# Kernel optimization log

Measured on AMD Instinct MI355X. Metric: run time of the kernel, lower is better.

The kernel has to match this reference:

```python
import jax, jax.numpy as jnp
import numpy as np


def setup_inputs() -> dict:
    key = jax.random.key(0)
    ks = jax.random.split(key, 8)
    B, C, H, W = 4, 256, 64, 64
    Ci = C // 8  # inter_channels = 32
    x = jax.random.normal(ks[0], (B, C, H, W), dtype=jnp.float32)
    # 1x1 conv weights stored as [out, in] matrices (kernel size 1)
    sq = 1.0 / np.sqrt(C)
    Wq = jax.random.uniform(ks[1], (Ci, C), jnp.float32, -sq, sq)
    bq = jax.random.uniform(ks[2], (Ci,), jnp.float32, -sq, sq)
    Wk = jax.random.uniform(ks[3], (Ci, C), jnp.float32, -sq, sq)
    bk = jax.random.uniform(ks[4], (Ci,), jnp.float32, -sq, sq)
    Wv = jax.random.uniform(ks[5], (C, C), jnp.float32, -sq, sq)
    bv = jax.random.uniform(ks[6], (C,), jnp.float32, -sq, sq)
    # torch initializes gamma to zeros; use a nonzero value so output depends on attention path
    gamma = jnp.array([0.5], dtype=jnp.float32)
    return {"x": x, "Wq": Wq, "bq": bq, "Wk": Wk, "bk": bk, "Wv": Wv, "bv": bv, "gamma": gamma}


def reference(x, Wq, bq, Wk, bk, Wv, bv, gamma):
    B, C, H, W = x.shape
    N = H * W
    xf = x.reshape(B, C, N)                        # [B, C, N]
    # 1x1 convs == channel-mixing matmuls
    q = jnp.einsum('oc,bcn->bon', Wq, xf) + bq[None, :, None]   # [B, Ci, N]
    k = jnp.einsum('oc,bcn->bon', Wk, xf) + bk[None, :, None]   # [B, Ci, N]
    v = jnp.einsum('oc,bcn->bon', Wv, xf) + bv[None, :, None]   # [B, C,  N]
    # energy[b, n, m] = sum_c q[b, c, n] * k[b, c, m]  (no scaling, per DANet)
    energy = jnp.einsum('bcn,bcm->bnm', q, k)      # [B, N, N]
    attention = jax.nn.softmax(energy, axis=-1)    # softmax over keys m
    # out[b, c, n] = sum_m v[b, c, m] * attention[b, n, m]
    out = jnp.einsum('bcm,bnm->bcn', v, attention)
    out = out.reshape(B, C, H, W)
    return gamma[0] * out + x
```

## Files before the change

kernel.cpp:

```cpp
#include <hip/hip_runtime.h>
#include <hip/hip_bf16.h>
#include <math.h>

typedef __bf16 bf16x8 __attribute__((ext_vector_type(8)));
typedef float  floatx4 __attribute__((ext_vector_type(4)));
typedef float  floatx16 __attribute__((ext_vector_type(16)));
typedef unsigned u32x2 __attribute__((ext_vector_type(2)));

#define MFMA(a, b, c)   __builtin_amdgcn_mfma_f32_16x16x32_bf16((a), (b), (c), 0, 0, 0)
#define MFMA32(a, b, c) __builtin_amdgcn_mfma_f32_32x32x16_bf16((a), (b), (c), 0, 0, 0)

__device__ __forceinline__ unsigned short f2bf(float f) {
  union { float f; unsigned u; } v; v.f = f;
  unsigned r = v.u + 0x7FFFu + ((v.u >> 16) & 1u);
  return (unsigned short)(r >> 16);
}
__device__ __forceinline__ float bf2f(unsigned short u) {
  union { unsigned u; float f; } v; v.u = ((unsigned)u) << 16;
  return v.f;
}
__device__ __forceinline__ unsigned pack2(float a, float b) {
  __bf16 x = (__bf16)a, y = (__bf16)b;
  unsigned short ux = __builtin_bit_cast(unsigned short, x);
  unsigned short uy = __builtin_bit_cast(unsigned short, y);
  return (unsigned)ux | ((unsigned)uy << 16);
}
__device__ __forceinline__ float exp2_fast(float x) {
#if __has_builtin(__builtin_amdgcn_exp2f)
  return __builtin_amdgcn_exp2f(x);
#else
  return exp2f(x);
#endif
}

__global__ __launch_bounds__(256) void k_wconv(const float* __restrict__ Wq,
                                               const float* __restrict__ Wk,
                                               const float* __restrict__ Wv,
                                               unsigned short* __restrict__ Wall) {
  int i = blockIdx.x * 256 + threadIdx.x;
  int o = i >> 8, c = i & 255;
  float v = (o < 32) ? Wq[o * 256 + c]
          : (o < 64) ? Wk[(o - 32) * 256 + c]
                     : Wv[(o - 64) * 256 + c];
  Wall[i] = f2bf(v);
}

__global__ __launch_bounds__(256) void k_xpose(const float* __restrict__ x,
                                               unsigned short* __restrict__ xT) {
  int bid = blockIdx.x;
  int b = bid >> 8, rem = bid & 255;
  int nb = rem >> 2, cb = rem & 3;
  int n0 = nb * 64, c0 = cb * 64;
  int tid = threadIdx.x;
  __shared__ alignas(16) unsigned short T[64][72];
#pragma unroll
  for (int i = 0; i < 4; ++i) {
    int idx = tid + 256 * i;
    int r = idx >> 4, g = idx & 15;
    float4 d = *(const float4*)(x + ((size_t)b * 256 + c0 + r) * 4096 + n0 + g * 4);
    T[g * 4 + 0][r] = f2bf(d.x);
    T[g * 4 + 1][r] = f2bf(d.y);
    T[g * 4 + 2][r] = f2bf(d.z);
    T[g * 4 + 3][r] = f2bf(d.w);
  }
  __syncthreads();
#pragma unroll
  for (int i = 0; i < 2; ++i) {
    int idx = tid + 256 * i;
    int j = idx >> 3, g = idx & 7;
    *(uint4*)(xT + ((size_t)b * 4096 + n0 + j) * 256 + c0 + g * 8) =
        *(const uint4*)&T[j][g * 8];
  }
}

__global__ __launch_bounds__(64, 4) void k_proj(const unsigned short* __restrict__ xT,
                                                const unsigned short* __restrict__ Wall,
                                                const float* __restrict__ bq,
                                                const float* __restrict__ bk,
                                                const float* __restrict__ bv,
                                                unsigned short* __restrict__ qbf,
                                                unsigned short* __restrict__ kbf,
                                                unsigned short* __restrict__ vbf) {
  int b = blockIdx.x >> 9;
  int m0 = ((blockIdx.x >> 1) & 255) * 16;
  int h = blockIdx.x & 1;
  int lane = threadIdx.x & 63;
  int l15 = lane & 15, quad = lane >> 4;

  floatx4 acc[10];
#pragma unroll
  for (int tt = 0; tt < 10; ++tt) acc[tt] = floatx4{0.f, 0.f, 0.f, 0.f};

  const unsigned short* arow = xT + ((size_t)b * 4096 + m0 + l15) * 256;
#pragma unroll
  for (int ks = 0; ks < 8; ++ks) {
    bf16x8 a = *(const bf16x8*)(arow + ks * 32 + quad * 8);
#pragma unroll
    for (int tt = 0; tt < 10; ++tt) {
      int gt = (tt < 2) ? (h * 2 + tt) : (4 + h * 8 + (tt - 2));
      bf16x8 w = *(const bf16x8*)(Wall + (size_t)(gt * 16 + l15) * 256 + ks * 32 + quad * 8);
      acc[tt] = MFMA(a, w, acc[tt]);
    }
  }
#pragma unroll
  for (int tt = 0; tt < 2; ++tt) {
    int o = (h * 2 + tt) * 16 + l15;
    float bias = (o < 32) ? bq[o] : bk[o - 32];
    float scale = (o < 32) ? 1.44269504088896340736f : 1.0f;
    unsigned short* dst = (o < 32) ? qbf : kbf;
    int oc = o & 31;
    int kh = oc >> 4, h2 = (oc >> 3) & 1, c8 = oc & 7;
#pragma unroll
    for (int r = 0; r < 4; ++r) {
      int m = m0 + quad * 4 + r;
      dst[(size_t)b * 131072 + (size_t)(m >> 5) * 1024 + kh * 512 + h2 * 256 +
          (m & 31) * 8 + c8] = f2bf((acc[tt][r] + bias) * scale);
    }
  }
  __shared__ alignas(16) unsigned short Os[128][24];
#pragma unroll
  for (int tt = 2; tt < 10; ++tt) {
    int lr = (tt - 2) * 16 + l15;
    int c = h * 128 + lr;
    float bias = bv[c];
#pragma unroll
    for (int r = 0; r < 4; ++r)
      Os[lr][quad * 4 + r] = f2bf(acc[tt][r] + bias);
  }
  __syncthreads();
  {
    int kb = m0 >> 5, kk = (m0 >> 4) & 1;
#pragma unroll
    for (int i = 0; i < 4; ++i) {
      int idx = threadIdx.x + 64 * i;
      int cbl = idx >> 6;
      int rem = idx & 63;
      int h2 = rem >> 5, ch = rem & 31;
      int r = cbl * 32 + ch;
      *(uint4*)(vbf + (size_t)b * 1048576 + (size_t)kb * 8192 +
                (size_t)(h * 4 + cbl) * 1024 + kk * 512 + h2 * 256 + ch * 8) =
          *(const uint4*)&Os[r][h2 * 8];
    }
  }
}

__device__ __forceinline__ void softmax_pack(floatx16 st, float& lp, bf16x8 (&pa)[2], int hi) {
  float p[16];
#pragma unroll
  for (int r = 0; r < 16; ++r) p[r] = exp2_fast(st[r]);
  lp += (((p[0] + p[1]) + (p[2] + p[3])) + ((p[4] + p[5]) + (p[6] + p[7]))) +
        (((p[8] + p[9]) + (p[10] + p[11])) + ((p[12] + p[13]) + (p[14] + p[15])));
  unsigned d0[4], d1[4];
#pragma unroll
  for (int t = 0; t < 4; ++t) {
    d0[t] = pack2(p[4 * t + 0], p[4 * t + 1]);
    d1[t] = pack2(p[4 * t + 2], p[4 * t + 3]);
  }
#pragma unroll
  for (int ks = 0; ks < 2; ++ks) {
#if __has_builtin(__builtin_amdgcn_permlane32_swap)
    (void)hi;
    u32x2 r0 = __builtin_amdgcn_permlane32_swap(d0[2 * ks], d0[2 * ks + 1], false, false);
    u32x2 r1 = __builtin_amdgcn_permlane32_swap(d1[2 * ks], d1[2 * ks + 1], false, false);
    union { unsigned u[4]; bf16x8 v; } u;
    u.u[0] = r0[0]; u.u[1] = r1[0]; u.u[2] = r0[1]; u.u[3] = r1[1];
    pa[ks] = u.v;
#else
    unsigned s0 = hi ? d0[2 * ks] : d0[2 * ks + 1];
    unsigned s1 = hi ? d1[2 * ks] : d1[2 * ks + 1];
    unsigned o0 = (unsigned)__shfl_xor((int)s0, 32);
    unsigned o1 = (unsigned)__shfl_xor((int)s1, 32);
    union { unsigned u[4]; bf16x8 v; } u;
    u.u[0] = hi ? o0 : d0[2 * ks];
    u.u[1] = hi ? o1 : d1[2 * ks];
    u.u[2] = hi ? d0[2 * ks + 1] : o0;
    u.u[3] = hi ? d1[2 * ks + 1] : o1;
    pa[ks] = u.v;
#endif
  }
}

__global__ __launch_bounds__(64, 2) void k_attn(const unsigned short* __restrict__ qbf,
                                                const unsigned short* __restrict__ kbf,
                                                const unsigned short* __restrict__ vbf,
                                                unsigned short* __restrict__ Obf,
                                                float* __restrict__ lsum) {
  int wg = (blockIdx.x & 7) * 256 + (blockIdx.x >> 3);
  const int qb = wg & 63;
  const int g  = wg >> 6;
  const int cw = g & 1;
  const int s  = (g >> 1) & 3;
  const int b  = g >> 3;
  const int lane = threadIdx.x & 63;
  const int l31 = lane & 31;
  const int hi  = lane >> 5;
  const int q0  = qb * 64;

  const floatx16 z16 = {0.f, 0.f, 0.f, 0.f, 0.f, 0.f, 0.f, 0.f,
                        0.f, 0.f, 0.f, 0.f, 0.f, 0.f, 0.f, 0.f};

  bf16x8 qf[2][2];
  {
    const unsigned short* qbase =
        qbf + (size_t)b * 131072 + (size_t)(qb * 2) * 1024 + hi * 256 + l31 * 8;
#pragma unroll
    for (int qs2 = 0; qs2 < 2; ++qs2)
#pragma unroll
      for (int kh = 0; kh < 2; ++kh)
        qf[qs2][kh] = *(const bf16x8*)(qbase + qs2 * 1024 + kh * 512);
  }

  floatx16 acc[2][4];
#pragma unroll
  for (int i = 0; i < 2; ++i)
#pragma unroll
    for (int j = 0; j < 4; ++j) acc[i][j] = z16;

  float lp0 = 0.f, lp1 = 0.f;

  const unsigned short* krow =
      kbf + (size_t)b * 131072 + (size_t)(s * 32) * 1024 + hi * 256 + l31 * 8;
  const unsigned short* vrow =
      vbf + (size_t)b * 1048576 + (size_t)(s * 32) * 8192 + (size_t)(cw * 4) * 1024 +
      hi * 256 + l31 * 8;

  bf16x8 kf0 = *(const bf16x8*)krow;
  bf16x8 kf1 = *(const bf16x8*)(krow + 512);
  floatx16 st0 = MFMA32(kf0, qf[0][0], z16);
  st0 = MFMA32(kf1, qf[0][1], st0);
  floatx16 st1 = MFMA32(kf0, qf[1][0], z16);
  st1 = MFMA32(kf1, qf[1][1], st1);
  kf0 = *(const bf16x8*)(krow + 1024);
  kf1 = *(const bf16x8*)(krow + 1024 + 512);

  for (int it = 0; it < 32; ++it) {
    bf16x8 vb[4][2];
    const unsigned short* vit = vrow + (size_t)it * 8192;
#pragma unroll
    for (int ct = 0; ct < 4; ++ct) {
      vb[ct][0] = *(const bf16x8*)(vit + ct * 1024);
      vb[ct][1] = *(const bf16x8*)(vit + ct * 1024 + 512);
    }

    bf16x8 pa[2][2];
    softmax_pack(st0, lp0, pa[0], hi);
    softmax_pack(st1, lp1, pa[1], hi);

    st0 = MFMA32(kf0, qf[0][0], z16);
    st0 = MFMA32(kf1, qf[0][1], st0);
    st1 = MFMA32(kf0, qf[1][0], z16);
    st1 = MFMA32(kf1, qf[1][1], st1);

    const unsigned short* kn = krow + (size_t)((it + 2) & 31) * 1024;
    kf0 = *(const bf16x8*)kn;
    kf1 = *(const bf16x8*)(kn + 512);

    __builtin_amdgcn_s_setprio(1);
#pragma unroll
    for (int ct = 0; ct < 4; ++ct) {
      acc[0][ct] = MFMA32(pa[0][0], vb[ct][0], acc[0][ct]);
      acc[1][ct] = MFMA32(pa[1][0], vb[ct][0], acc[1][ct]);
      acc[0][ct] = MFMA32(pa[0][1], vb[ct][1], acc[0][ct]);
      acc[1][ct] = MFMA32(pa[1][1], vb[ct][1], acc[1][ct]);
    }
    __builtin_amdgcn_s_setprio(0);
  }

  lp0 += __shfl_xor(lp0, 32);
  lp1 += __shfl_xor(lp1, 32);
  if (cw == 0) {
    float lv = hi ? lp1 : lp0;
    lsum[((size_t)s * 4 + b) * 4096 + q0 + hi * 32 + l31] = lv;
  }
#pragma unroll
  for (int qs2 = 0; qs2 < 2; ++qs2)
#pragma unroll
    for (int ct = 0; ct < 4; ++ct) {
      unsigned short* orow = Obf +
          (((size_t)s * 4 + b) * 256 + cw * 128 + ct * 32 + l31) * 4096 +
          q0 + qs2 * 32 + hi * 4;
#pragma unroll
      for (int gi = 0; gi < 4; ++gi) {
        unsigned w0 = pack2(acc[qs2][ct][4 * gi + 0], acc[qs2][ct][4 * gi + 1]);
        unsigned w1 = pack2(acc[qs2][ct][4 * gi + 2], acc[qs2][ct][4 * gi + 3]);
        unsigned long long w = (unsigned long long)w0 | ((unsigned long long)w1 << 32);
        *(unsigned long long*)(orow + 8 * gi) = w;
      }
    }
}

__global__ __launch_bounds__(256) void k_merge(const unsigned short* __restrict__ Obf,
                                               const float* __restrict__ lsum,
                                               const float* __restrict__ x,
                                               const float* __restrict__ gma,
                                               float* __restrict__ out) {
  int t = blockIdx.x * 256 + threadIdx.x;
  int n4 = t & 1023;
  int c = (t >> 10) & 255;
  int b = t >> 18;
  int n = n4 << 2;
  size_t xa = (((size_t)b * 256 + c) << 12) + n;
  float4 xv = *(const float4*)(x + xa);
  float L0 = 0.f, L1 = 0.f, L2 = 0.f, L3 = 0.f;
  float o0 = 0.f, o1 = 0.f, o2 = 0.f, o3 = 0.f;
#pragma unroll
  for (int s = 0; s < 4; ++s) {
    float4 ls = *(const float4*)(lsum + (((size_t)s * 4 + b) << 12) + n);
    L0 += ls.x; L1 += ls.y; L2 += ls.z; L3 += ls.w;
    ushort4 ov = *(const ushort4*)(Obf + ((((size_t)s * 4 + b) * 256 + c) << 12) + n);
    o0 += bf2f(ov.x); o1 += bf2f(ov.y); o2 += bf2f(ov.z); o3 += bf2f(ov.w);
  }
  float g = gma[0];
  float4 r;
  r.x = xv.x + g * o0 / L0;
  r.y = xv.y + g * o1 / L1;
  r.z = xv.z + g * o2 / L2;
  r.w = xv.w + g * o3 / L3;
  *(float4*)(out + xa) = r;
}

extern "C" void kernel_launch(void* const* d_in, const int* in_sizes, int n_in,
                              void* d_out, int out_size, void* d_ws, size_t ws_size,
                              hipStream_t stream) {
  const float* x   = (const float*)d_in[0];
  const float* Wq  = (const float*)d_in[1];
  const float* bq  = (const float*)d_in[2];
  const float* Wk  = (const float*)d_in[3];
  const float* bk  = (const float*)d_in[4];
  const float* Wv  = (const float*)d_in[5];
  const float* bv  = (const float*)d_in[6];
  const float* gma = (const float*)d_in[7];
  float* out = (float*)d_out;

  unsigned short* qbf  = (unsigned short*)d_ws;
  unsigned short* kbf  = qbf + (size_t)4 * 131072;
  unsigned short* vbf  = kbf + (size_t)4 * 131072;
  unsigned short* Wall = vbf + (size_t)4 * 1048576;
  unsigned short* xT   = Wall + (size_t)320 * 256;
  unsigned short* Obf  = xT;
  float* lsum = (float*)(Obf + (size_t)4 * 4 * 256 * 4096);

  k_wconv<<<320, 256, 0, stream>>>(Wq, Wk, Wv, Wall);
  k_xpose<<<1024, 256, 0, stream>>>(x, xT);
  k_proj<<<2048, 64, 0, stream>>>(xT, Wall, bq, bk, bv, qbf, kbf, vbf);
  k_attn<<<2048, 64, 0, stream>>>(qbf, kbf, vbf, Obf, lsum);
  k_merge<<<4096, 256, 0, stream>>>(Obf, lsum, x, gma, out);
}
```

Before: 169.4 us.

## Fuse input transpose into projection kernel via shared-memory staging

Removes the separate transpose kernel that wrote a bf16 transposed copy of x to global memory. The projection kernel now loads a 16-position strip of x across all 256 channels directly, converts it to bf16 in shared memory, and uses four waves per block, each computing one q/k tile and four v tiles. This saves a kernel launch and a global write and read of the transposed input. The cost is that global reads of x are 64-byte strided per channel row, which coalesce poorly, and shared-memory writes during the transpose may bank-conflict.

Result: no change. 168.7 us (-0.4%).

```diff
diff --git a/kernel.cpp b/kernel.cpp
--- a/kernel.cpp
+++ b/kernel.cpp
@@ -45,66 +45,57 @@
   Wall[i] = f2bf(v);
 }
 
-__global__ __launch_bounds__(256) void k_xpose(const float* __restrict__ x,
-                                               unsigned short* __restrict__ xT) {
-  int bid = blockIdx.x;
-  int b = bid >> 8, rem = bid & 255;
-  int nb = rem >> 2, cb = rem & 3;
-  int n0 = nb * 64, c0 = cb * 64;
+__global__ __launch_bounds__(256) void k_projx(const float* __restrict__ x,
+                                               const unsigned short* __restrict__ Wall,
+                                               const float* __restrict__ bq,
+                                               const float* __restrict__ bk,
+                                               const float* __restrict__ bv,
+                                               unsigned short* __restrict__ qbf,
+                                               unsigned short* __restrict__ kbf,
+                                               unsigned short* __restrict__ vbf) {
+  int b = blockIdx.x >> 8;
+  int m0 = (blockIdx.x & 255) * 16;
   int tid = threadIdx.x;
-  __shared__ alignas(16) unsigned short T[64][72];
-#pragma unroll
-  for (int i = 0; i < 4; ++i) {
-    int idx = tid + 256 * i;
-    int r = idx >> 4, g = idx & 15;
-    float4 d = *(const float4*)(x + ((size_t)b * 256 + c0 + r) * 4096 + n0 + g * 4);
-    T[g * 4 + 0][r] = f2bf(d.x);
-    T[g * 4 + 1][r] = f2bf(d.y);
-    T[g * 4 + 2][r] = f2bf(d.z);
-    T[g * 4 + 3][r] = f2bf(d.w);
+  int qr = tid >> 6;
+  int lane = tid & 63;
+  int l15 = lane & 15, quad = lane >> 4;
+
+  __shared__ alignas(16) unsigned short xs[16][264];
+  __shared__ alignas(16) unsigned short Os[4][64][24];
+
+  {
+    const float* xrow = x + ((size_t)b * 256 + tid) * 4096 + m0;
+#pragma unroll
+    for (int g = 0; g < 4; ++g) {
+      float4 d = *(const float4*)(xrow + g * 4);
+      xs[g * 4 + 0][tid] = f2bf(d.x);
+      xs[g * 4 + 1][tid] = f2bf(d.y);
+      xs[g * 4 + 2][tid] = f2bf(d.z);
+      xs[g * 4 + 3][tid] = f2bf(d.w);
+    }
   }
   __syncthreads();
-#pragma unroll
-  for (int i = 0; i < 2; ++i) {
-    int idx = tid + 256 * i;
-    int j = idx >> 3, g = idx & 7;
-    *(uint4*)(xT + ((size_t)b * 4096 + n0 + j) * 256 + c0 + g * 8) =
-        *(const uint4*)&T[j][g * 8];
-  }
-}
-
-__global__ __launch_bounds__(64, 4) void k_proj(const unsigned short* __restrict__ xT,
-                                                const unsigned short* __restrict__ Wall,
-                                                const float* __restrict__ bq,
-                                                const float* __restrict__ bk,
-                                                const float* __restrict__ bv,
-                                                unsigned short* __restrict__ qbf,
-                                                unsigned short* __restrict__ kbf,
-                                                unsigned short* __restrict__ vbf) {
-  int b = blockIdx.x >> 9;
-  int m0 = ((blockIdx.x >> 1) & 255) * 16;
-  int h = blockIdx.x & 1;
-  int lane = threadIdx.x & 63;
-  int l15 = lane & 15, quad = lane >> 4;
-
-  floatx4 acc[10];
-#pragma unroll
-  for (int tt = 0; tt < 10; ++tt) acc[tt] = floatx4{0.f, 0.f, 0.f, 0.f};
-
-  const unsigned short* arow = xT + ((size_t)b * 4096 + m0 + l15) * 256;
+
+  floatx4 acc[5];
+#pragma unroll
+  for (int tt = 0; tt < 5; ++tt) acc[tt] = floatx4{0.f, 0.f, 0.f, 0.f};
+
 #pragma unroll
   for (int ks = 0; ks < 8; ++ks) {
-    bf16x8 a = *(const bf16x8*)(arow + ks * 32 + quad * 8);
-#pragma unroll
-    for (int tt = 0; tt < 10; ++tt) {
-      int gt = (tt < 2) ? (h * 2 + tt) : (4 + h * 8 + (tt - 2));
+    bf16x8 a = *(const bf16x8*)&xs[l15][ks * 32 + quad * 8];
+    {
+      bf16x8 w = *(const bf16x8*)(Wall + (size_t)(qr * 16 + l15) * 256 + ks * 32 + quad * 8);
+      acc[0] = MFMA(a, w, acc[0]);
+    }
+#pragma unroll
+    for (int t = 0; t < 4; ++t) {
+      int gt = 4 + qr * 4 + t;
       bf16x8 w = *(const bf16x8*)(Wall + (size_t)(gt * 16 + l15) * 256 + ks * 32 + quad * 8);
-      acc[tt] = MFMA(a, w, acc[tt]);
-    }
-  }
-#pragma unroll
-  for (int tt = 0; tt < 2; ++tt) {
-    int o = (h * 2 + tt) * 16 + l15;
+      acc[1 + t] = MFMA(a, w, acc[1 + t]);
+    }
+  }
+  {
+    int o = qr * 16 + l15;
     float bias = (o < 32) ? bq[o] : bk[o - 32];
     float scale = (o < 32) ? 1.44269504088896340736f : 1.0f;
     unsigned short* dst = (o < 32) ? qbf : kbf;
@@ -114,32 +105,30 @@
     for (int r = 0; r < 4; ++r) {
       int m = m0 + quad * 4 + r;
       dst[(size_t)b * 131072 + (size_t)(m >> 5) * 1024 + kh * 512 + h2 * 256 +
-          (m & 31) * 8 + c8] = f2bf((acc[tt][r] + bias) * scale);
-    }
-  }
-  __shared__ alignas(16) unsigned short Os[128][24];
-#pragma unroll
-  for (int tt = 2; tt < 10; ++tt) {
-    int lr = (tt - 2) * 16 + l15;
-    int c = h * 128 + lr;
+          (m & 31) * 8 + c8] = f2bf((acc[0][r] + bias) * scale);
+    }
+  }
+#pragma unroll
+  for (int t = 0; t < 4; ++t) {
+    int lr = t * 16 + l15;
+    int c = qr * 64 + lr;
     float bias = bv[c];
 #pragma unroll
     for (int r = 0; r < 4; ++r)
-      Os[lr][quad * 4 + r] = f2bf(acc[tt][r] + bias);
+      Os[qr][lr][quad * 4 + r] = f2bf(acc[1 + t][r] + bias);
   }
   __syncthreads();
   {
     int kb = m0 >> 5, kk = (m0 >> 4) & 1;
 #pragma unroll
-    for (int i = 0; i < 4; ++i) {
-      int idx = threadIdx.x + 64 * i;
-      int cbl = idx >> 6;
-      int rem = idx & 63;
-      int h2 = rem >> 5, ch = rem & 31;
-      int r = cbl * 32 + ch;
+    for (int i = 0; i < 2; ++i) {
+      int idx = lane + 64 * i;
+      int r = idx >> 1, g = idx & 1;
+      int c = qr * 64 + r;
+      int cb = c >> 5, ch = c & 31;
       *(uint4*)(vbf + (size_t)b * 1048576 + (size_t)kb * 8192 +
-                (size_t)(h * 4 + cbl) * 1024 + kk * 512 + h2 * 256 + ch * 8) =
-          *(const uint4*)&Os[r][h2 * 8];
+                (size_t)cb * 1024 + kk * 512 + g * 256 + ch * 8) =
+          *(const uint4*)&Os[qr][r][g * 8];
     }
   }
 }
@@ -336,13 +325,11 @@
   unsigned short* kbf  = qbf + (size_t)4 * 131072;
   unsigned short* vbf  = kbf + (size_t)4 * 131072;
   unsigned short* Wall = vbf + (size_t)4 * 1048576;
-  unsigned short* xT   = Wall + (size_t)320 * 256;
-  unsigned short* Obf  = xT;
+  unsigned short* Obf  = Wall + (size_t)320 * 256;
   float* lsum = (float*)(Obf + (size_t)4 * 4 * 256 * 4096);
 
   k_wconv<<<320, 256, 0, stream>>>(Wq, Wk, Wv, Wall);
-  k_xpose<<<1024, 256, 0, stream>>>(x, xT);
-  k_proj<<<2048, 64, 0, stream>>>(xT, Wall, bq, bk, bv, qbf, kbf, vbf);
+  k_projx<<<1024, 256, 0, stream>>>(x, Wall, bq, bk, bv, qbf, kbf, vbf);
   k_attn<<<2048, 64, 0, stream>>>(qbf, kbf, vbf, Obf, lsum);
   k_merge<<<4096, 256, 0, stream>>>(Obf, lsum, x, gma, out);
 }
```
